# Kernel optimization log

Hardware: AMD Instinct MI355X
Metric: run time of the kernel (lower is better)

Reference implementation:

```python
import jax, jax.numpy as jnp
import numpy as np

B, T, S, F, D, M = 8, 8192, 8192, 64, 64, 128
EPS = 1e-9


def _draw_omega(n_omega, d_feature, rng):
    # Stacked orthogonal blocks scaled by sqrt(d_feature), as in the TF module.
    n_blocks = (n_omega + d_feature - 1) // d_feature + 1
    blocks = []
    for _ in range(n_blocks):
        g = rng.standard_normal((d_feature, d_feature)).astype(np.float32)
        q, _ = np.linalg.qr(g)
        blocks.append(q * np.sqrt(float(d_feature)))
    return jnp.asarray(np.concatenate(blocks, axis=0)[:n_omega])


def setup_inputs() -> dict:
    k0 = jax.random.key(0)
    kq, kv, kk = jax.random.split(k0, 3)
    query = jax.random.normal(kq, (B, T, F), dtype=jnp.float32)
    value = jax.random.normal(kv, (B, S, D), dtype=jnp.float32)
    key = jax.random.normal(kk, (B, S, F), dtype=jnp.float32)
    omega = _draw_omega(M, F, np.random.default_rng(0))  # (M, F)
    return {"query": query, "value": value, "key": key, "omega": omega}


def _phi(x, omega):
    # x: (B, L, F) -> (B, L, 2M) positive random features
    m = omega.shape[0]
    square_sum = jnp.sum(x * x, axis=-1, keepdims=True) / 2.0  # (B, L, 1)
    xw = jnp.einsum('blf,mf->blm', x, omega)                   # (B, L, M)
    unnorm = jnp.exp(jnp.concatenate([xw, -xw], axis=-1) - square_sum) + EPS
    return unnorm / jnp.sqrt(2.0 * m)


def reference(query, value, key, omega):
    q = _phi(query, omega)  # (B, T, 2M)
    k = _phi(key, omega)    # (B, S, 2M)
    ones = jnp.ones(value.shape[:-1] + (1,), dtype=value.dtype)
    v1 = jnp.concatenate([value, ones], axis=-1)               # (B, S, D+1)
    kv = jnp.einsum('bsm,bsd->bmd', k, v1)                     # (B, 2M, D+1)
    qkv = jnp.einsum('btm,bmd->btd', q, kv)                    # (B, T, D+1)
    normalizer = qkv[:, :, -1:]
    return qkv[:, :, :-1] / normalizer
```

## Files before the change

kernel.cpp:

```cpp
#include <hip/hip_runtime.h>


constexpr int NB = 8;
constexpr int NT = 8192;
constexpr float EPSF = 1e-9f;
constexpr float SCALE = 0.0625f;

typedef short s8v __attribute__((ext_vector_type(8)));
typedef short s4v __attribute__((ext_vector_type(4)));
typedef float f4v __attribute__((ext_vector_type(4)));

__device__ inline f4v mfma16(s8v a, s8v b, f4v c) {
  return __builtin_amdgcn_mfma_f32_16x16x32_bf16(a, b, c, 0, 0, 0);
}

__device__ inline short bf16_rne(float f) {
  unsigned u = __builtin_bit_cast(unsigned, f);
  u += 0x7fffu + ((u >> 16) & 1u);
  return (short)(u >> 16);
}
__device__ inline float bf16_to_f(short h) {
  unsigned u = ((unsigned)(unsigned short)h) << 16;
  return __builtin_bit_cast(float, u);
}

__global__ void setup_omega(const float* __restrict__ omega,
                            short* __restrict__ ohf, short* __restrict__ olf) {
  int i = blockIdx.x * 256 + threadIdx.x;
  if (i >= 128 * 64) return;
  int jj = i & 7;
  int lane = (i >> 3) & 63;
  int h = (i >> 9) & 1;
  int ft = i >> 10;
  int m = ft * 16 + (lane & 15);
  int f = h * 32 + (lane >> 4) * 8 + jj;
  float wv = omega[m * 64 + f];
  short hh = bf16_rne(wv);
  ohf[i] = hh;
  olf[i] = bf16_rne(wv - bf16_to_f(hh));
}

struct PhiRows {
  s8v ah0, al0, ah1, al1;
  float ssr[4];
  float ss;
};

__device__ inline void split8(f4v a, f4v b, s8v& h, s8v& l) {
  float v[8] = {a.x, a.y, a.z, a.w, b.x, b.y, b.z, b.w};
#pragma unroll
  for (int j = 0; j < 8; ++j) {
    short hh = bf16_rne(v[j]);
    h[j] = hh;
    l[j] = bf16_rne(v[j] - bf16_to_f(hh));
  }
}

__device__ inline void load_phi_rows(const float* __restrict__ xrow_base, int lane, PhiRows& P) {
  const int r = lane & 15, q = lane >> 4;
  const float* p = xrow_base + r * 64 + q * 8;
  f4v u0 = *(const f4v*)(p);
  f4v u1 = *(const f4v*)(p + 4);
  f4v u2 = *(const f4v*)(p + 32);
  f4v u3 = *(const f4v*)(p + 36);
  float ss = u0.x * u0.x + u0.y * u0.y + u0.z * u0.z + u0.w * u0.w
           + u1.x * u1.x + u1.y * u1.y + u1.z * u1.z + u1.w * u1.w
           + u2.x * u2.x + u2.y * u2.y + u2.z * u2.z + u2.w * u2.w
           + u3.x * u3.x + u3.y * u3.y + u3.z * u3.z + u3.w * u3.w;
  ss += __shfl_xor(ss, 16, 64);
  ss += __shfl_xor(ss, 32, 64);
  ss *= 0.5f;
  P.ss = ss;
#pragma unroll
  for (int reg = 0; reg < 4; ++reg) P.ssr[reg] = __shfl(ss, q * 4 + reg, 64);
  split8(u0, u1, P.ah0, P.al0);
  split8(u2, u3, P.ah1, P.al1);
}

__device__ inline f4v phi_xw_tile(const PhiRows& P, const short* __restrict__ ohf,
                                  const short* __restrict__ olf, int ft, int lane) {
  const int o0 = ft * 1024 + lane * 8;
  s8v bh0 = *(const s8v*)(ohf + o0);
  s8v bh1 = *(const s8v*)(ohf + o0 + 512);
  s8v bl0 = *(const s8v*)(olf + o0);
  s8v bl1 = *(const s8v*)(olf + o0 + 512);
  f4v c = {0.f, 0.f, 0.f, 0.f};
  c = mfma16(P.ah0, bh0, c);
  c = mfma16(P.ah1, bh1, c);
  c = mfma16(P.al0, bh0, c);
  c = mfma16(P.al1, bh1, c);
  c = mfma16(P.ah0, bl0, c);
  c = mfma16(P.ah1, bl1, c);
  return c;
}

__device__ inline f4v phi_xw_tile_T(const PhiRows& P, const short* __restrict__ ohf,
                                    const short* __restrict__ olf, int ft, int lane) {
  const int o0 = ft * 1024 + lane * 8;
  s8v ah0 = *(const s8v*)(ohf + o0);
  s8v ah1 = *(const s8v*)(ohf + o0 + 512);
  s8v al0 = *(const s8v*)(olf + o0);
  s8v al1 = *(const s8v*)(olf + o0 + 512);
  f4v c = {0.f, 0.f, 0.f, 0.f};
  c = mfma16(ah0, P.ah0, c);
  c = mfma16(ah1, P.ah1, c);
  c = mfma16(al0, P.ah0, c);
  c = mfma16(al1, P.ah1, c);
  c = mfma16(ah0, P.al0, c);
  c = mfma16(ah1, P.al1, c);
  return c;
}

constexpr int KF_P = 72;
constexpr int QF_P = 264;
constexpr int PART_P = 72;
constexpr int PART_SZ = 256 * PART_P;
constexpr int KV_GRID = 1024;

__global__ __launch_bounds__(256, 4) void kv_fused(
    const float* __restrict__ key, const float* __restrict__ value,
    const short* __restrict__ ohf, const short* __restrict__ olf,
    short* __restrict__ partial, float* __restrict__ kvacc, int use_partial) {
  __shared__ short kft[4 * 64 * KF_P];
  const int tid = threadIdx.x, lane = tid & 63, w = tid >> 6;
  const int b = blockIdx.x >> 7;
  const int s0 = (blockIdx.x & 127) * 64;
  const int q = lane >> 4, r15 = lane & 15;
  short* kw = kft + w * 64 * KF_P;

  s8v vone;
#pragma unroll
  for (int jj = 0; jj < 8; ++jj) vone[jj] = (r15 == 0) ? (short)0x3F80 : (short)0;

#pragma unroll
  for (int rg = 0; rg < 4; ++rg) {
    PhiRows P;
    load_phi_rows(key + ((size_t)b * NT + s0 + rg * 16) * 64, lane, P);
#pragma unroll
    for (int ftl = 0; ftl < 2; ++ftl) {
      f4v c = phi_xw_tile(P, ohf, olf, w * 2 + ftl, lane);
      s4v pk, nk;
#pragma unroll
      for (int reg = 0; reg < 4; ++reg) {
        float xw = c[reg];
        pk[reg] = bf16_rne((__expf(xw - P.ssr[reg]) + EPSF) * SCALE);
        nk[reg] = bf16_rne((__expf(-xw - P.ssr[reg]) + EPSF) * SCALE);
      }
      *(s4v*)(kw + (ftl * 16 + r15) * KF_P + rg * 16 + q * 4) = pk;
      *(s4v*)(kw + (32 + ftl * 16 + r15) * KF_P + rg * 16 + q * 4) = nk;
    }
  }
  f4v acc[4][5];
#pragma unroll
  for (int mt = 0; mt < 4; ++mt)
#pragma unroll
    for (int n = 0; n < 5; ++n) acc[mt][n] = f4v{0.f, 0.f, 0.f, 0.f};
  const float* vb = value + ((size_t)b * NT + s0) * 64;
#pragma unroll
  for (int ks = 0; ks < 2; ++ks) {
    s8v bf[5];
#pragma unroll
    for (int n = 0; n < 4; ++n) {
#pragma unroll
      for (int jj = 0; jj < 8; ++jj)
        bf[n][jj] = bf16_rne(vb[(ks * 32 + q * 8 + jj) * 64 + n * 16 + r15]);
    }
    bf[4] = vone;
#pragma unroll
    for (int mt = 0; mt < 4; ++mt) {
      s8v a = *(const s8v*)(kw + (mt * 16 + r15) * KF_P + ks * 32 + q * 8);
#pragma unroll
      for (int n = 0; n < 5; ++n) acc[mt][n] = mfma16(a, bf[n], acc[mt][n]);
    }
  }
  if (use_partial) {
#pragma unroll
    for (int mt = 0; mt < 4; ++mt) {
#pragma unroll
      for (int n = 0; n < 4; ++n) {
#pragma unroll
        for (int reg = 0; reg < 4; ++reg)
          kw[(mt * 16 + q * 4 + reg) * KF_P + n * 16 + r15] = bf16_rne(acc[mt][n][reg]);
      }
      if (r15 == 0) {
#pragma unroll
        for (int reg = 0; reg < 4; ++reg)
          kw[(mt * 16 + q * 4 + reg) * KF_P + 64] = bf16_rne(acc[mt][4][reg]);
      }
    }
    short* pb = partial + (size_t)blockIdx.x * PART_SZ + w * 64 * PART_P;
#pragma unroll
    for (int i = 0; i < 9; ++i) {
      int e = i * 64 + lane;
      *(s8v*)(pb + e * 8) = *(const s8v*)(kw + e * 8);
    }
  } else {
    float* pb = kvacc + (size_t)b * PART_SZ;
#pragma unroll
    for (int mt = 0; mt < 4; ++mt) {
#pragma unroll
      for (int reg = 0; reg < 4; ++reg) {
        int ml = mt * 16 + q * 4 + reg;
        int m = (ml < 32) ? (w * 32 + ml) : (128 + w * 32 + (ml - 32));
#pragma unroll
        for (int n = 0; n < 4; ++n)
          atomicAdd(pb + (size_t)m * PART_P + n * 16 + r15, acc[mt][n][reg]);
        if (r15 == 0) atomicAdd(pb + (size_t)m * PART_P + 64, acc[mt][4][reg]);
      }
    }
  }
}

__global__ __launch_bounds__(256) void kv_finalize(
    const short* __restrict__ partial, const float* __restrict__ kvacc,
    short* __restrict__ kvfrag, int use_partial) {
  int i = blockIdx.x * 256 + threadIdx.x;
  int b = i / 20480;
  int rem = i - b * 20480;
  int m = rem / 80;
  int d = rem - m * 80;
  float s = 0.f;
  if (d < 65) {
    if (use_partial) {
      int w_, ml;
      if (m < 128) { w_ = m >> 5; ml = m & 31; }
      else { int mm = m - 128; w_ = mm >> 5; ml = 32 + (mm & 31); }
      int pr = w_ * 64 + ml;
      const short* p = partial + (size_t)(b * 128) * PART_SZ + pr * PART_P + d;
#pragma unroll 8
      for (int c = 0; c < 128; ++c) s += bf16_to_f(p[(size_t)c * PART_SZ]);
    } else {
      s = kvacc[(size_t)b * PART_SZ + (size_t)m * PART_P + d];
    }
  }
  int ks = m >> 5, qq = (m >> 3) & 3, j = m & 7;
  int n = d >> 4, r = d & 15;
  int lane = qq * 16 + r;
  if (d < 80)
    kvfrag[(((size_t)b * 40 + ks * 5 + n) * 64 + lane) * 8 + j] = bf16_rne(s);
}

__global__ __launch_bounds__(256, 4) void qkv_fused(
    const float* __restrict__ query, const short* __restrict__ ohf,
    const short* __restrict__ olf, const short* __restrict__ kvfrag,
    float* __restrict__ out) {
  __shared__ __align__(16) short qf[64 * QF_P];
  const int tid = threadIdx.x, lane = tid & 63, w = tid >> 6;
  const int b = blockIdx.x >> 7;
  const int t0 = (blockIdx.x & 127) * 64;
  const int q = lane >> 4, r15 = lane & 15;

  {
    PhiRows P;
    load_phi_rows(query + ((size_t)b * NT + t0 + w * 16) * 64, lane, P);
    const int t_loc = w * 16 + r15;
#pragma unroll
    for (int ft = 0; ft < 8; ++ft) {
      f4v c = phi_xw_tile_T(P, ohf, olf, ft, lane);
      s4v pk, nk;
#pragma unroll
      for (int reg = 0; reg < 4; ++reg) {
        float xw = c[reg];
        pk[reg] = bf16_rne((__expf(xw - P.ss) + EPSF) * SCALE);
        nk[reg] = bf16_rne((__expf(-xw - P.ss) + EPSF) * SCALE);
      }
      *(s4v*)(qf + t_loc * QF_P + ft * 16 + q * 4) = pk;
      *(s4v*)(qf + t_loc * QF_P + 128 + ft * 16 + q * 4) = nk;
    }
  }
  f4v acc[5];
#pragma unroll
  for (int n = 0; n < 5; ++n) acc[n] = f4v{0.f, 0.f, 0.f, 0.f};
  const short* kvb = kvfrag + (size_t)b * 40 * 512;
#pragma unroll
  for (int ks = 0; ks < 8; ++ks) {
    s8v a = *(const s8v*)(qf + (w * 16 + r15) * QF_P + ks * 32 + q * 8);
#pragma unroll
    for (int n = 0; n < 5; ++n) {
      s8v bf = *(const s8v*)(kvb + ((size_t)(ks * 5 + n)) * 512 + lane * 8);
      acc[n] = mfma16(a, bf, acc[n]);
    }
  }
  float den_r[4];
#pragma unroll
  for (int reg = 0; reg < 4; ++reg) den_r[reg] = __shfl(acc[4][reg], lane & 48, 64);
  float* stg = (float*)(qf + w * 16 * QF_P);
#pragma unroll
  for (int n = 0; n < 4; ++n)
#pragma unroll
    for (int reg = 0; reg < 4; ++reg) {
      int row = q * 4 + reg;
      int col = n * 16 + r15;
      stg[row * 68 + col] = acc[n][reg] / den_r[reg];
    }
  float* ob = out + ((size_t)b * NT + t0 + w * 16) * 64;
#pragma unroll
  for (int rr = 0; rr < 4; ++rr) {
    int row = rr * 4 + q;
    int c4 = r15 * 4;
    *(f4v*)(ob + row * 64 + c4) = *(const f4v*)(stg + row * 68 + c4);
  }
}

extern "C" void kernel_launch(void* const* d_in, const int* in_sizes, int n_in,
                              void* d_out, int out_size, void* d_ws, size_t ws_size,
                              hipStream_t stream) {
  const float* query = (const float*)d_in[0];
  const float* value = (const float*)d_in[1];
  const float* key   = (const float*)d_in[2];
  const float* omega = (const float*)d_in[3];
  float* out = (float*)d_out;

  char* ws = (char*)d_ws;
  short* ohf = (short*)ws;
  short* olf = (short*)(ws + 16384);
  short* kvfrag = (short*)(ws + 32768);
  short* partial = (short*)(ws + 360448);
  float* kvacc = (float*)(ws + 360448);
  const size_t need_full = 360448 + (size_t)KV_GRID * PART_SZ * 2;
  const int use_partial = (ws_size >= need_full) ? 1 : 0;

  setup_omega<<<32, 256, 0, stream>>>(omega, ohf, olf);
  if (!use_partial) {
    hipMemsetAsync(kvacc, 0, (size_t)8 * PART_SZ * 4, stream);
  }
  kv_fused<<<KV_GRID, 256, 0, stream>>>(key, value, ohf, olf, partial, kvacc, use_partial);
  kv_finalize<<<640, 256, 0, stream>>>(partial, kvacc, kvfrag, use_partial);
  qkv_fused<<<1024, 256, 0, stream>>>(query, ohf, olf, kvfrag, out);
}
```

Baseline: 135.0 us.

## Split kv_fused blocks by feature half and double sequence chunk per block

Each kv_fused block now handles only the positive or the negative half of the random features (selected by block index) and loops over two 64-row sequence chunks instead of one. This halves LDS use, accumulator registers and the partial buffer per block. It also halves the number of partials kv_finalize must reduce per output element, cutting partial-buffer traffic. In exchange, the key projection (xw) is recomputed by both halves, so the key loads and omega MFMAs are duplicated.

```diff
diff --git a/kernel.cpp b/kernel.cpp
--- a/kernel.cpp
+++ b/kernel.cpp
@@ -114,68 +114,75 @@
 constexpr int KF_P = 72;
 constexpr int QF_P = 264;
 constexpr int PART_P = 72;
-constexpr int PART_SZ = 256 * PART_P;
+constexpr int PART_ROWS = 128;
+constexpr int PART_SZ = PART_ROWS * PART_P;
+constexpr int ACC_SZ = 256 * PART_P;
 constexpr int KV_GRID = 1024;
 
 __global__ __launch_bounds__(256, 4) void kv_fused(
     const float* __restrict__ key, const float* __restrict__ value,
     const short* __restrict__ ohf, const short* __restrict__ olf,
     short* __restrict__ partial, float* __restrict__ kvacc, int use_partial) {
-  __shared__ short kft[4 * 64 * KF_P];
+  __shared__ short kft[4 * 32 * KF_P];
   const int tid = threadIdx.x, lane = tid & 63, w = tid >> 6;
   const int b = blockIdx.x >> 7;
-  const int s0 = (blockIdx.x & 127) * 64;
+  const int rem = blockIdx.x & 127;
+  const int scb = rem >> 1, mh = rem & 1;
+  const int s00 = scb * 128;
   const int q = lane >> 4, r15 = lane & 15;
-  short* kw = kft + w * 64 * KF_P;
+  short* kw = kft + w * 32 * KF_P;
 
   s8v vone;
 #pragma unroll
   for (int jj = 0; jj < 8; ++jj) vone[jj] = (r15 == 0) ? (short)0x3F80 : (short)0;
 
-#pragma unroll
-  for (int rg = 0; rg < 4; ++rg) {
-    PhiRows P;
-    load_phi_rows(key + ((size_t)b * NT + s0 + rg * 16) * 64, lane, P);
-#pragma unroll
-    for (int ftl = 0; ftl < 2; ++ftl) {
-      f4v c = phi_xw_tile(P, ohf, olf, w * 2 + ftl, lane);
-      s4v pk, nk;
-#pragma unroll
-      for (int reg = 0; reg < 4; ++reg) {
-        float xw = c[reg];
-        pk[reg] = bf16_rne((__expf(xw - P.ssr[reg]) + EPSF) * SCALE);
-        nk[reg] = bf16_rne((__expf(-xw - P.ssr[reg]) + EPSF) * SCALE);
-      }
-      *(s4v*)(kw + (ftl * 16 + r15) * KF_P + rg * 16 + q * 4) = pk;
-      *(s4v*)(kw + (32 + ftl * 16 + r15) * KF_P + rg * 16 + q * 4) = nk;
-    }
-  }
-  f4v acc[4][5];
-#pragma unroll
-  for (int mt = 0; mt < 4; ++mt)
+  f4v acc[2][5];
+#pragma unroll
+  for (int mt = 0; mt < 2; ++mt)
 #pragma unroll
     for (int n = 0; n < 5; ++n) acc[mt][n] = f4v{0.f, 0.f, 0.f, 0.f};
-  const float* vb = value + ((size_t)b * NT + s0) * 64;
-#pragma unroll
-  for (int ks = 0; ks < 2; ++ks) {
-    s8v bf[5];
-#pragma unroll
-    for (int n = 0; n < 4; ++n) {
-#pragma unroll
-      for (int jj = 0; jj < 8; ++jj)
-        bf[n][jj] = bf16_rne(vb[(ks * 32 + q * 8 + jj) * 64 + n * 16 + r15]);
-    }
-    bf[4] = vone;
-#pragma unroll
-    for (int mt = 0; mt < 4; ++mt) {
-      s8v a = *(const s8v*)(kw + (mt * 16 + r15) * KF_P + ks * 32 + q * 8);
-#pragma unroll
-      for (int n = 0; n < 5; ++n) acc[mt][n] = mfma16(a, bf[n], acc[mt][n]);
+
+  for (int sc = 0; sc < 2; ++sc) {
+    const int s0 = s00 + sc * 64;
+#pragma unroll 2
+    for (int rg = 0; rg < 4; ++rg) {
+      PhiRows P;
+      load_phi_rows(key + ((size_t)b * NT + s0 + rg * 16) * 64, lane, P);
+#pragma unroll
+      for (int tl = 0; tl < 2; ++tl) {
+        f4v c = phi_xw_tile(P, ohf, olf, w * 2 + tl, lane);
+        s4v pk;
+#pragma unroll
+        for (int reg = 0; reg < 4; ++reg) {
+          float xw = c[reg];
+          float arg = mh ? (-xw - P.ssr[reg]) : (xw - P.ssr[reg]);
+          pk[reg] = bf16_rne((__expf(arg) + EPSF) * SCALE);
+        }
+        *(s4v*)(kw + (tl * 16 + r15) * KF_P + rg * 16 + q * 4) = pk;
+      }
+    }
+    const float* vb = value + ((size_t)b * NT + s0) * 64;
+#pragma unroll
+    for (int ks = 0; ks < 2; ++ks) {
+      s8v bf[5];
+#pragma unroll
+      for (int n = 0; n < 4; ++n) {
+#pragma unroll
+        for (int jj = 0; jj < 8; ++jj)
+          bf[n][jj] = bf16_rne(vb[(ks * 32 + q * 8 + jj) * 64 + n * 16 + r15]);
+      }
+      bf[4] = vone;
+#pragma unroll
+      for (int mt = 0; mt < 2; ++mt) {
+        s8v a = *(const s8v*)(kw + (mt * 16 + r15) * KF_P + ks * 32 + q * 8);
+#pragma unroll
+        for (int n = 0; n < 5; ++n) acc[mt][n] = mfma16(a, bf[n], acc[mt][n]);
+      }
     }
   }
   if (use_partial) {
 #pragma unroll
-    for (int mt = 0; mt < 4; ++mt) {
+    for (int mt = 0; mt < 2; ++mt) {
 #pragma unroll
       for (int n = 0; n < 4; ++n) {
 #pragma unroll
@@ -188,20 +195,19 @@
           kw[(mt * 16 + q * 4 + reg) * KF_P + 64] = bf16_rne(acc[mt][4][reg]);
       }
     }
-    short* pb = partial + (size_t)blockIdx.x * PART_SZ + w * 64 * PART_P;
+    short* pb = partial + (size_t)blockIdx.x * PART_SZ + w * 32 * PART_P;
 #pragma unroll
     for (int i = 0; i < 9; ++i) {
       int e = i * 64 + lane;
-      *(s8v*)(pb + e * 8) = *(const s8v*)(kw + e * 8);
+      *(s4v*)(pb + e * 4) = *(const s4v*)(kw + e * 4);
     }
   } else {
-    float* pb = kvacc + (size_t)b * PART_SZ;
-#pragma unroll
-    for (int mt = 0; mt < 4; ++mt) {
+    float* pb = kvacc + (size_t)b * ACC_SZ;
+#pragma unroll
+    for (int mt = 0; mt < 2; ++mt) {
 #pragma unroll
       for (int reg = 0; reg < 4; ++reg) {
-        int ml = mt * 16 + q * 4 + reg;
-        int m = (ml < 32) ? (w * 32 + ml) : (128 + w * 32 + (ml - 32));
+        int m = mh * 128 + w * 32 + mt * 16 + q * 4 + reg;
 #pragma unroll
         for (int n = 0; n < 4; ++n)
           atomicAdd(pb + (size_t)m * PART_P + n * 16 + r15, acc[mt][n][reg]);
@@ -222,15 +228,12 @@
   float s = 0.f;
   if (d < 65) {
     if (use_partial) {
-      int w_, ml;
-      if (m < 128) { w_ = m >> 5; ml = m & 31; }
-      else { int mm = m - 128; w_ = mm >> 5; ml = 32 + (mm & 31); }
-      int pr = w_ * 64 + ml;
-      const short* p = partial + (size_t)(b * 128) * PART_SZ + pr * PART_P + d;
+      int mh = m >> 7, pr = m & 127;
+      const short* p = partial + ((size_t)(b * 128 + mh)) * PART_SZ + pr * PART_P + d;
 #pragma unroll 8
-      for (int c = 0; c < 128; ++c) s += bf16_to_f(p[(size_t)c * PART_SZ]);
+      for (int c = 0; c < 64; ++c) s += bf16_to_f(p[(size_t)c * 2 * PART_SZ]);
     } else {
-      s = kvacc[(size_t)b * PART_SZ + (size_t)m * PART_P + d];
+      s = kvacc[(size_t)b * ACC_SZ + (size_t)m * PART_P + d];
     }
   }
   int ks = m >> 5, qq = (m >> 3) & 3, j = m & 7;
@@ -322,7 +325,7 @@
 
   setup_omega<<<32, 256, 0, stream>>>(omega, ohf, olf);
   if (!use_partial) {
-    hipMemsetAsync(kvacc, 0, (size_t)8 * PART_SZ * 4, stream);
+    hipMemsetAsync(kvacc, 0, (size_t)8 * ACC_SZ * 4, stream);
   }
   kv_fused<<<KV_GRID, 256, 0, stream>>>(key, value, ohf, olf, partial, kvacc, use_partial);
   kv_finalize<<<640, 256, 0, stream>>>(partial, kvacc, kvfrag, use_partial);
```

Measured after the change: 194.9 us. 44.4% more time.
